# Performance work log

Hardware: AMD Instinct MI355X
Metric: run time of the kernel (lower is better)

Reference implementation:

```python
import jax, jax.numpy as jnp
import numpy as np

EMBED_DIM = 768
N_HEADS = 12
MLP_HID = 3072  # mlp_ratio 4.0
LN_EPS = 1e-6


def setup_inputs() -> dict:
    key = jax.random.key(0)
    ks = jax.random.split(key, 12)
    B, N, C = 4, 2048, EMBED_DIM
    s = 0.02
    return {
        "x": jax.random.normal(ks[0], (B, N, C), jnp.float32),
        "mask": jnp.ones((B, N), jnp.int32),
        "ln1_g": jnp.ones((C,), jnp.float32),
        "ln1_b": jnp.zeros((C,), jnp.float32),
        "qkv_w": jax.random.normal(ks[1], (C, 3 * C), jnp.float32) * s,
        "qkv_b": jnp.zeros((3 * C,), jnp.float32),
        "proj_w": jax.random.normal(ks[2], (C, C), jnp.float32) * s,
        "proj_b": jnp.zeros((C,), jnp.float32),
        "ln2_g": jnp.ones((C,), jnp.float32),
        "ln2_b": jnp.zeros((C,), jnp.float32),
        "fc1_w": jax.random.normal(ks[3], (C, MLP_HID), jnp.float32) * s,
        "fc1_b": jnp.zeros((MLP_HID,), jnp.float32),
        "fc2_w": jax.random.normal(ks[4], (MLP_HID, C), jnp.float32) * s,
        "fc2_b": jnp.zeros((C,), jnp.float32),
    }


def _layernorm(x, g, b):
    mu = jnp.mean(x, axis=-1, keepdims=True)
    var = jnp.mean(jnp.square(x - mu), axis=-1, keepdims=True)
    return (x - mu) * jax.lax.rsqrt(var + LN_EPS) * g + b


def _block(x, mask, ln1_g, ln1_b, qkv_w, qkv_b, proj_w, proj_b,
           ln2_g, ln2_b, fc1_w, fc1_b, fc2_w, fc2_b):
    B, N, C = x.shape
    H, D = N_HEADS, C // N_HEADS
    scale = D ** -0.5

    # --- attention (pre-norm) ---
    h = _layernorm(x, ln1_g, ln1_b)
    qkv = h @ qkv_w + qkv_b                      # [B,N,3C]
    qkv = qkv.reshape(B, N, 3, H, D).transpose(2, 0, 3, 1, 4)
    q, k, v = qkv[0], qkv[1], qkv[2]             # [B,H,N,D]
    scores = jnp.einsum("bhqd,bhkd->bhqk", q, k * scale)
    # 2-D mask path: (bsz, seq) -> (bsz, 1, seq, 1), mask queries
    m = mask[:, None, :, None]
    scores = jnp.where(m == 0, jnp.finfo(scores.dtype).min, scores)
    attn = jax.nn.softmax(scores, axis=-1)
    vals = jnp.einsum("bhqk,bhkd->bhqd", attn, v)
    vals = vals.transpose(0, 2, 1, 3).reshape(B, N, C)
    x = x + (vals @ proj_w + proj_b)

    # --- MLP (pre-norm, GELU exact) ---
    h = _layernorm(x, ln2_g, ln2_b)
    h = jax.nn.gelu(h @ fc1_w + fc1_b, approximate=False)
    x = x + (h @ fc2_w + fc2_b)
    return x


def reference(x, mask, ln1_g, ln1_b, qkv_w, qkv_b, proj_w, proj_b,
              ln2_g, ln2_b, fc1_w, fc1_b, fc2_w, fc2_b):
    return _block(x, mask, ln1_g, ln1_b, qkv_w, qkv_b, proj_w, proj_b,
                  ln2_g, ln2_b, fc1_w, fc1_b, fc2_w, fc2_b)
```

## Files before the change

### kernel.cpp

```cpp
#include <hip/hip_runtime.h>
#include <hip/hip_bf16.h>
#include <math.h>

using bf16 = __hip_bfloat16;
typedef short s16x8 __attribute__((ext_vector_type(8)));
typedef float f32x4 __attribute__((ext_vector_type(4)));
typedef float f32x16 __attribute__((ext_vector_type(16)));

#define LOG2E 1.4426950408889634f
#define QSCALE 0.18033688f

__device__ inline unsigned short f2bf(float f) {
    bf16 h = __float2bfloat16(f);
    return __builtin_bit_cast(unsigned short, h);
}

__device__ inline void gload_lds16(const void* g, void* l) {
    __builtin_amdgcn_global_load_lds(
        (const __attribute__((address_space(1))) void*)g,
        (__attribute__((address_space(3))) void*)l, 16, 0, 0);
}

__device__ inline float swap_halves(float x, int hi) {
    unsigned a = __builtin_bit_cast(unsigned, x);
    unsigned b = a;
    asm volatile("v_permlane32_swap_b32 %0, %1" : "+v"(a), "+v"(b));
    return hi ? __builtin_bit_cast(float, a) : __builtin_bit_cast(float, b);
}

__device__ inline unsigned cvtpk(float lo, float hi) {
    unsigned r;
    asm("v_cvt_pk_bf16_f32 %0, %1, %2" : "=v"(r) : "v"(lo), "v"(hi));
    return r;
}

__device__ inline s16x8 build_pfrag(float p0, float p1, float p2, float p3,
                                    float p4, float p5, float p6, float p7) {
    unsigned w01 = cvtpk(p0, p1);
    unsigned w23 = cvtpk(p2, p3);
    unsigned w45 = cvtpk(p4, p5);
    unsigned w67 = cvtpk(p6, p7);
    asm volatile("v_permlane32_swap_b32 %0, %1" : "+v"(w01), "+v"(w45));
    asm volatile("v_permlane32_swap_b32 %0, %1" : "+v"(w23), "+v"(w67));
    int4 t = {(int)w01, (int)w23, (int)w45, (int)w67};
    return __builtin_bit_cast(s16x8, t);
}

__global__ __launch_bounds__(256) void transpose_bf16(
    const float* __restrict__ in, bf16* __restrict__ out, int K, int N)
{
    __shared__ float tile[32][33];
    const int bx = blockIdx.x * 32;
    const int by = blockIdx.y * 32;
    const int tx = threadIdx.x, ty = threadIdx.y;
    #pragma unroll
    for (int i = 0; i < 32; i += 8)
        tile[ty + i][tx] = in[(size_t)(by + ty + i) * N + bx + tx];
    __syncthreads();
    #pragma unroll
    for (int i = 0; i < 32; i += 8)
        out[(size_t)(bx + ty + i) * K + by + tx] = __float2bfloat16(tile[tx][ty + i]);
}

__global__ __launch_bounds__(256) void ln_kernel(
    const float* __restrict__ x, const float* __restrict__ g,
    const float* __restrict__ bb, bf16* __restrict__ out)
{
    const int row = blockIdx.x;
    const float* xr = x + (size_t)row * 768;
    float v[3];
    float s = 0.f, s2 = 0.f;
    #pragma unroll
    for (int i = 0; i < 3; ++i) {
        v[i] = xr[threadIdx.x + i * 256];
        s += v[i];
        s2 += v[i] * v[i];
    }
    #pragma unroll
    for (int off = 1; off < 64; off <<= 1) {
        s += __shfl_xor(s, off);
        s2 += __shfl_xor(s2, off);
    }
    __shared__ float rs[4], rs2[4];
    const int wave = threadIdx.x >> 6;
    if ((threadIdx.x & 63) == 0) { rs[wave] = s; rs2[wave] = s2; }
    __syncthreads();
    s = rs[0] + rs[1] + rs[2] + rs[3];
    s2 = rs2[0] + rs2[1] + rs2[2] + rs2[3];
    const float mu = s * (1.f / 768.f);
    const float var = s2 * (1.f / 768.f) - mu * mu;
    const float r = rsqrtf(var + 1e-6f);
    bf16* orow = out + (size_t)row * 768;
    #pragma unroll
    for (int i = 0; i < 3; ++i) {
        const int col = threadIdx.x + i * 256;
        orow[col] = __float2bfloat16((v[i] - mu) * r * g[col] + bb[col]);
    }
}

#define BM 128
#define BN 128
#define BK 64

template <int EPI>
__global__ __launch_bounds__(256) void gemm_bt(
    const bf16* __restrict__ A, const bf16* __restrict__ Bt,
    const float* __restrict__ bias, const float* __restrict__ resid,
    void* __restrict__ outp, const int* __restrict__ mask,
    bf16* __restrict__ Qb, bf16* __restrict__ Kb, bf16* __restrict__ Vt,
    int M, int N, int K)
{
    __shared__ alignas(16) char smem[32768];
    char* As = smem;
    char* Bs = smem + 16384;
    const int tid = threadIdx.x;
    const int lane = tid & 63;
    const int wave = tid >> 6;
    const int wm = wave >> 1, wn = wave & 1;
    const int lr = lane & 15, lg = lane >> 4;
    const int bm = blockIdx.x, bn = blockIdx.y;

    f32x4 acc[4][4] = {};

    const size_t a_row0 = (size_t)bm * BM;
    const size_t b_row0 = (size_t)bn * BN;

    for (int kt = 0; kt < K; kt += BK) {
        #pragma unroll
        for (int i = 0; i < 4; ++i) {
            const int id = tid + i * 256;
            const int row = id >> 3, c = id & 7;
            const int cs = (c ^ (row & 7)) * 8;
            gload_lds16(A + (a_row0 + row) * K + kt + cs, As + id * 16);
            gload_lds16(Bt + (b_row0 + row) * K + kt + cs, Bs + id * 16);
        }
        __syncthreads();
        #pragma unroll
        for (int ks = 0; ks < 2; ++ks) {
            s16x8 af[4], bfr[4];
            #pragma unroll
            for (int mf = 0; mf < 4; ++mf) {
                const int row = wm * 64 + mf * 16 + lr;
                const int c = ks * 4 + lg;
                af[mf] = *reinterpret_cast<const s16x8*>(As + row * 128 + ((c ^ (row & 7)) * 16));
            }
            #pragma unroll
            for (int nf = 0; nf < 4; ++nf) {
                const int row = wn * 64 + nf * 16 + lr;
                const int c = ks * 4 + lg;
                bfr[nf] = *reinterpret_cast<const s16x8*>(Bs + row * 128 + ((c ^ (row & 7)) * 16));
            }
            #pragma unroll
            for (int mf = 0; mf < 4; ++mf)
                #pragma unroll
                for (int nf = 0; nf < 4; ++nf)
                    acc[mf][nf] = __builtin_amdgcn_mfma_f32_16x16x32_bf16(
                        af[mf], bfr[nf], acc[mf][nf], 0, 0, 0);
        }
        __syncthreads();
    }

    if (EPI == 3) {
        const int rq = bn / 6;
        const int bb_ = bm >> 4;
        if (rq == 2) {
            char* Ws = smem + wave * 8192;
            #pragma unroll
            for (int nf = 0; nf < 4; ++nf) {
                const int cl = nf * 16 + lr;
                const int gn = bn * 128 + wn * 64 + nf * 16 + lr;
                const float bs = bias[gn];
                #pragma unroll
                for (int mf = 0; mf < 4; ++mf) {
                    unsigned short pk[4];
                    #pragma unroll
                    for (int i = 0; i < 4; ++i) pk[i] = f2bf(acc[mf][nf][i] + bs);
                    const int slot = (2 * mf + (lg >> 1)) ^ (cl & 7);
                    *reinterpret_cast<long long*>(Ws + cl * 128 + slot * 16 + (lg & 1) * 8) =
                        *reinterpret_cast<const long long*>(pk);
                }
            }
            __syncthreads();
            const int nb = (bm * 128 + wm * 64) & 2047;
            const int cb = (bn - 12) * 128 + wn * 64;
            #pragma unroll
            for (int r = 0; r < 8; ++r) {
                const int cl = r * 8 + (lane >> 3);
                const int j = lane & 7;
                const int4 vv = *reinterpret_cast<const int4*>(
                    Ws + cl * 128 + ((j ^ (cl & 7)) * 16));
                const int c = cb + cl;
                const int hh = c >> 6, dd = c & 63;
                *reinterpret_cast<int4*>(
                    Vt + ((size_t)(bb_ * 12 + hh) * 64 + dd) * 2048 + nb + j * 8) = vv;
            }
        } else {
            const int cb = bn * 128 - rq * 768 + wn * 64;
            bf16* dst = (rq == 0) ? Qb : Kb;
            #pragma unroll
            for (int mf = 0; mf < 4; ++mf) {
                #pragma unroll
                for (int i = 0; i < 4; ++i) {
                    const int gm = bm * 128 + wm * 64 + mf * 16 + 4 * lg + i;
                    const int n = gm & 2047;
                    const float msc = (rq == 0) ? (mask[gm] ? QSCALE : 0.f) : 1.f;
                    #pragma unroll
                    for (int nf = 0; nf < 4; ++nf) {
                        const int c = cb + nf * 16 + lr;
                        const int h = c >> 6, d = c & 63;
                        const int gn = bn * 128 + wn * 64 + nf * 16 + lr;
                        const float v = (acc[mf][nf][i] + bias[gn]) * msc;
                        dst[((size_t)(bb_ * 12 + h) * 2048 + n) * 64 + d] =
                            __float2bfloat16(v);
                    }
                }
            }
        }
        return;
    }

    #pragma unroll
    for (int mf = 0; mf < 4; ++mf) {
        #pragma unroll
        for (int i = 0; i < 4; ++i) {
            const int gm = bm * BM + wm * 64 + mf * 16 + 4 * lg + i;
            #pragma unroll
            for (int nf = 0; nf < 4; ++nf) {
                const int gn = bn * BN + wn * 64 + nf * 16 + lr;
                float v = acc[mf][nf][i] + bias[gn];
                if (EPI == 1) v += resid[(size_t)gm * N + gn];
                if (EPI == 2) {
                    const float x3 = v * v * v;
                    const float z = fmaf(x3, 0.044715f, v) * 2.3022080f;
                    const float e = __builtin_amdgcn_exp2f(z);
                    v = v - v * __builtin_amdgcn_rcpf(1.f + e);
                }
                if (EPI == 1)
                    reinterpret_cast<float*>(outp)[(size_t)gm * N + gn] = v;
                else
                    reinterpret_cast<bf16*>(outp)[(size_t)gm * N + gn] = __float2bfloat16(v);
            }
        }
    }
}

__global__ __launch_bounds__(256, 3) void attn_kernel(
    const bf16* __restrict__ Qb, const bf16* __restrict__ Kb,
    const bf16* __restrict__ Vt, bf16* __restrict__ out)
{
    __shared__ alignas(16) char Ks[2][64 * 128];
    __shared__ alignas(16) char Vs[2][64 * 128];

    const int lin = blockIdx.x;
    const int xcd = lin & 7, slot = lin >> 3;
    const int pair = xcd * 6 + (slot >> 4);
    const int qb = slot & 15;
    const int b = pair / 12, h = pair % 12;

    const int tid = threadIdx.x, lane = tid & 63, wave = tid >> 6;
    const int lq = lane & 31;
    const int hi = lane >> 5;
    const size_t bh = (size_t)(b * 12 + h);
    const bf16* Kh = Kb + bh * 2048 * 64;
    const bf16* Vh = Vt + bh * 64 * 2048;
    const int q0w = qb * 128 + wave * 32;

    s16x8 qf[4];
    {
        const bf16* qp = Qb + (bh * 2048 + q0w + lq) * 64 + 8 * hi;
        #pragma unroll
        for (int ks = 0; ks < 4; ++ks)
            qf[ks] = *reinterpret_cast<const s16x8*>(qp + 16 * ks);
    }

    int sKoff0, sKoff1, dst0, dst1;
    size_t sVoff0, sVoff1;
    {
        const int id0 = tid;
        const int R0 = id0 >> 4;
        const int u0 = (id0 & 15) ^ (R0 & 15);
        const int rt0 = 2 * R0 + (u0 >> 3), s80 = (u0 & 7) * 8;
        sKoff0 = rt0 * 64 + s80;
        sVoff0 = (size_t)rt0 * 2048 + s80;
        dst0 = id0 * 16;
        const int id1 = tid + 256;
        const int R1 = id1 >> 4;
        const int u1 = (id1 & 15) ^ (R1 & 15);
        const int rt1 = 2 * R1 + (u1 >> 3), s81 = (u1 & 7) * 8;
        sKoff1 = rt1 * 64 + s81;
        sVoff1 = (size_t)rt1 * 2048 + s81;
        dst1 = id1 * 16;
    }

    const int rh = lq >> 1;
    const int m7 = rh & 7;
    const int rbase = rh * 256 + (((((lq & 1) << 3) ^ (rh & 8))) << 4);

    float l_r = 0.f;
    f32x16 o0 = {}, o1 = {};

    #define STAGE(buf, kb)                                                    \
        do {                                                                  \
            gload_lds16(Kh + (kb) * 4096 + sKoff0, Ks[buf] + dst0);           \
            gload_lds16(Vh + (kb) * 64 + sVoff0, Vs[buf] + dst0);             \
            gload_lds16(Kh + (kb) * 4096 + sKoff1, Ks[buf] + dst1);           \
            gload_lds16(Vh + (kb) * 64 + sVoff1, Vs[buf] + dst1);             \
        } while (0)

    STAGE(0, 0);
    __syncthreads();
    int cur = 0;

    for (int kb = 0; kb < 32; ++kb) {
        if (kb < 31) STAGE(cur ^ 1, kb + 1);
        const char* Kc = Ks[cur] + rbase;
        const char* Vc = Vs[cur] + rbase;

        f32x16 st0 = {}, st1 = {};
        __builtin_amdgcn_s_setprio(1);
        #pragma unroll
        for (int ks = 0; ks < 4; ++ks) {
            const int so = (((2 * ks + hi) ^ m7) << 4);
            const s16x8 kf0 = *reinterpret_cast<const s16x8*>(Kc + so);
            st0 = __builtin_amdgcn_mfma_f32_32x32x16_bf16(kf0, qf[ks], st0, 0, 0, 0);
            const s16x8 kf1 = *reinterpret_cast<const s16x8*>(Kc + 4096 + so);
            st1 = __builtin_amdgcn_mfma_f32_32x32x16_bf16(kf1, qf[ks], st1, 0, 0, 0);
        }
        __builtin_amdgcn_s_setprio(0);

        float p0[16], p1[16];
        float rsa = 0.f, rsb = 0.f;
        #pragma unroll
        for (int r = 0; r < 16; ++r) {
            p0[r] = __builtin_amdgcn_exp2f(st0[r]);
            p1[r] = __builtin_amdgcn_exp2f(st1[r]);
            rsa += p0[r];
            rsb += p1[r];
        }
        l_r += rsa + rsb;

        const s16x8 pf00 = build_pfrag(p0[0], p0[1], p0[2], p0[3], p0[4], p0[5], p0[6], p0[7]);
        const s16x8 pf01 = build_pfrag(p0[8], p0[9], p0[10], p0[11], p0[12], p0[13], p0[14], p0[15]);
        const s16x8 pf10 = build_pfrag(p1[0], p1[1], p1[2], p1[3], p1[4], p1[5], p1[6], p1[7]);
        const s16x8 pf11 = build_pfrag(p1[8], p1[9], p1[10], p1[11], p1[12], p1[13], p1[14], p1[15]);

        __builtin_amdgcn_s_setprio(1);
        #pragma unroll
        for (int kf4 = 0; kf4 < 4; ++kf4) {
            const s16x8 pf = (kf4 == 0) ? pf00 : (kf4 == 1) ? pf01
                           : (kf4 == 2) ? pf10 : pf11;
            const int so = (((2 * kf4 + hi) ^ m7) << 4);
            const s16x8 vf0 = *reinterpret_cast<const s16x8*>(Vc + so);
            o0 = __builtin_amdgcn_mfma_f32_32x32x16_bf16(vf0, pf, o0, 0, 0, 0);
            const s16x8 vf1 = *reinterpret_cast<const s16x8*>(Vc + 4096 + so);
            o1 = __builtin_amdgcn_mfma_f32_32x32x16_bf16(vf1, pf, o1, 0, 0, 0);
        }
        __builtin_amdgcn_s_setprio(0);

        __syncthreads();
        cur ^= 1;
    }
    #undef STAGE

    l_r += swap_halves(l_r, hi);

    const float rl = 1.0f / l_r;
    bf16* orow = out + (size_t)(b * 2048 + q0w + lq) * 768 + h * 64;
    #pragma unroll
    for (int g = 0; g < 4; ++g) {
        unsigned short pk0[4], pk1[4];
        #pragma unroll
        for (int i = 0; i < 4; ++i) {
            pk0[i] = f2bf(o0[4 * g + i] * rl);
            pk1[i] = f2bf(o1[4 * g + i] * rl);
        }
        const int d0 = 8 * g + 4 * hi;
        *reinterpret_cast<int2*>(orow + d0) = *reinterpret_cast<const int2*>(pk0);
        *reinterpret_cast<int2*>(orow + 32 + d0) = *reinterpret_cast<const int2*>(pk1);
    }
}

extern "C" void kernel_launch(void* const* d_in, const int* in_sizes, int n_in,
                              void* d_out, int out_size, void* d_ws, size_t ws_size,
                              hipStream_t stream)
{
    (void)in_sizes; (void)n_in; (void)out_size; (void)ws_size;
    const float* x      = (const float*)d_in[0];
    const int*   mask   = (const int*)d_in[1];
    const float* ln1_g  = (const float*)d_in[2];
    const float* ln1_b  = (const float*)d_in[3];
    const float* qkv_w  = (const float*)d_in[4];
    const float* qkv_b  = (const float*)d_in[5];
    const float* proj_w = (const float*)d_in[6];
    const float* proj_b = (const float*)d_in[7];
    const float* ln2_g  = (const float*)d_in[8];
    const float* ln2_b  = (const float*)d_in[9];
    const float* fc1_w  = (const float*)d_in[10];
    const float* fc1_b  = (const float*)d_in[11];
    const float* fc2_w  = (const float*)d_in[12];
    const float* fc2_b  = (const float*)d_in[13];
    float* out = (float*)d_out;
    char* ws = (char*)d_ws;

    bf16*  Wt_qkv  = (bf16*)(ws + 0);
    bf16*  Wt_proj = (bf16*)(ws + 3538944);
    bf16*  Wt_fc1  = (bf16*)(ws + 4718592);
    bf16*  Wt_fc2  = (bf16*)(ws + 9437184);
    bf16*  hbuf    = (bf16*)(ws + 14155776);
    bf16*  attnout = (bf16*)(ws + 64487424);
    float* x1      = (float*)(ws + 77070336);
    bf16*  h2      = (bf16*)(ws + 102236160);
    bf16*  a1      = (bf16*)(ws + 114819072);
    bf16*  Qb      = (bf16*)(ws + 114819072);
    bf16*  Kb      = (bf16*)(ws + 127401984);
    bf16*  Vt      = (bf16*)(ws + 139984896);

    const dim3 tb(32, 8);
    transpose_bf16<<<dim3(2304 / 32, 768 / 32), tb, 0, stream>>>(qkv_w, Wt_qkv, 768, 2304);
    transpose_bf16<<<dim3(768 / 32, 768 / 32), tb, 0, stream>>>(proj_w, Wt_proj, 768, 768);
    transpose_bf16<<<dim3(3072 / 32, 768 / 32), tb, 0, stream>>>(fc1_w, Wt_fc1, 768, 3072);
    transpose_bf16<<<dim3(768 / 32, 3072 / 32), tb, 0, stream>>>(fc2_w, Wt_fc2, 3072, 768);

    ln_kernel<<<8192, 256, 0, stream>>>(x, ln1_g, ln1_b, hbuf);
    gemm_bt<3><<<dim3(64, 18), 256, 0, stream>>>(hbuf, Wt_qkv, qkv_b, nullptr, nullptr,
                                                 mask, Qb, Kb, Vt, 8192, 2304, 768);
    attn_kernel<<<768, 256, 0, stream>>>(Qb, Kb, Vt, attnout);
    gemm_bt<1><<<dim3(64, 6), 256, 0, stream>>>(attnout, Wt_proj, proj_b, x, x1,
                                                nullptr, nullptr, nullptr, nullptr, 8192, 768, 768);
    ln_kernel<<<8192, 256, 0, stream>>>(x1, ln2_g, ln2_b, h2);
    gemm_bt<2><<<dim3(64, 24), 256, 0, stream>>>(h2, Wt_fc1, fc1_b, nullptr, a1,
                                                 nullptr, nullptr, nullptr, nullptr, 8192, 3072, 768);
    gemm_bt<1><<<dim3(64, 6), 256, 0, stream>>>(a1, Wt_fc2, fc2_b, x1, out,
                                                nullptr, nullptr, nullptr, nullptr, 8192, 768, 3072);
}
```

Baseline: 273.7 us.

## Use 64-row GEMM tiles for N=768 GEMMs, fuse transposes, MFMA row sums

```diff
diff --git a/kernel.cpp b/kernel.cpp
--- a/kernel.cpp
+++ b/kernel.cpp
@@ -19,13 +19,6 @@
     __builtin_amdgcn_global_load_lds(
         (const __attribute__((address_space(1))) void*)g,
         (__attribute__((address_space(3))) void*)l, 16, 0, 0);
-}
-
-__device__ inline float swap_halves(float x, int hi) {
-    unsigned a = __builtin_bit_cast(unsigned, x);
-    unsigned b = a;
-    asm volatile("v_permlane32_swap_b32 %0, %1" : "+v"(a), "+v"(b));
-    return hi ? __builtin_bit_cast(float, a) : __builtin_bit_cast(float, b);
 }
 
 __device__ inline unsigned cvtpk(float lo, float hi) {
@@ -46,12 +39,24 @@
     return __builtin_bit_cast(s16x8, t);
 }
 
-__global__ __launch_bounds__(256) void transpose_bf16(
-    const float* __restrict__ in, bf16* __restrict__ out, int K, int N)
+__global__ __launch_bounds__(256) void transpose_all(
+    const float* __restrict__ qkv_w, const float* __restrict__ proj_w,
+    const float* __restrict__ fc1_w, const float* __restrict__ fc2_w,
+    bf16* __restrict__ Wqkv, bf16* __restrict__ Wproj,
+    bf16* __restrict__ Wfc1, bf16* __restrict__ Wfc2)
 {
+    int t = blockIdx.x;
+    const float* in;
+    bf16* out;
+    int K, N, xt;
+    if (t < 1728)      { in = qkv_w;  out = Wqkv;  K = 768;  N = 2304; xt = 72; }
+    else if (t < 2304) { in = proj_w; out = Wproj; K = 768;  N = 768;  xt = 24; t -= 1728; }
+    else if (t < 4608) { in = fc1_w;  out = Wfc1;  K = 768;  N = 3072; xt = 96; t -= 2304; }
+    else               { in = fc2_w;  out = Wfc2;  K = 3072; N = 768;  xt = 24; t -= 4608; }
+    const int bx = (t % xt) * 32;
+    const int by = (t / xt) * 32;
+
     __shared__ float tile[32][33];
-    const int bx = blockIdx.x * 32;
-    const int by = blockIdx.y * 32;
     const int tx = threadIdx.x, ty = threadIdx.y;
     #pragma unroll
     for (int i = 0; i < 32; i += 8)
@@ -98,14 +103,10 @@
     }
 }
 
-#define BM 128
-#define BN 128
-#define BK 64
-
 template <int EPI>
 __global__ __launch_bounds__(256) void gemm_bt(
     const bf16* __restrict__ A, const bf16* __restrict__ Bt,
-    const float* __restrict__ bias, const float* __restrict__ resid,
+    const float* __restrict__ bias,
     void* __restrict__ outp, const int* __restrict__ mask,
     bf16* __restrict__ Qb, bf16* __restrict__ Kb, bf16* __restrict__ Vt,
     int M, int N, int K)
@@ -122,10 +123,10 @@
 
     f32x4 acc[4][4] = {};
 
-    const size_t a_row0 = (size_t)bm * BM;
-    const size_t b_row0 = (size_t)bn * BN;
-
-    for (int kt = 0; kt < K; kt += BK) {
+    const size_t a_row0 = (size_t)bm * 128;
+    const size_t b_row0 = (size_t)bn * 128;
+
+    for (int kt = 0; kt < K; kt += 64) {
         #pragma unroll
         for (int i = 0; i < 4; ++i) {
             const int id = tid + i * 256;
@@ -223,22 +224,93 @@
     for (int mf = 0; mf < 4; ++mf) {
         #pragma unroll
         for (int i = 0; i < 4; ++i) {
-            const int gm = bm * BM + wm * 64 + mf * 16 + 4 * lg + i;
+            const int gm = bm * 128 + wm * 64 + mf * 16 + 4 * lg + i;
             #pragma unroll
             for (int nf = 0; nf < 4; ++nf) {
-                const int gn = bn * BN + wn * 64 + nf * 16 + lr;
+                const int gn = bn * 128 + wn * 64 + nf * 16 + lr;
                 float v = acc[mf][nf][i] + bias[gn];
-                if (EPI == 1) v += resid[(size_t)gm * N + gn];
                 if (EPI == 2) {
                     const float x3 = v * v * v;
                     const float z = fmaf(x3, 0.044715f, v) * 2.3022080f;
                     const float e = __builtin_amdgcn_exp2f(z);
                     v = v - v * __builtin_amdgcn_rcpf(1.f + e);
                 }
-                if (EPI == 1)
-                    reinterpret_cast<float*>(outp)[(size_t)gm * N + gn] = v;
-                else
-                    reinterpret_cast<bf16*>(outp)[(size_t)gm * N + gn] = __float2bfloat16(v);
+                reinterpret_cast<bf16*>(outp)[(size_t)gm * N + gn] = __float2bfloat16(v);
+            }
+        }
+    }
+}
+
+__global__ __launch_bounds__(256) void gemm64(
+    const bf16* __restrict__ A, const bf16* __restrict__ Bt,
+    const float* __restrict__ bias, const float* __restrict__ resid,
+    float* __restrict__ outp, int M, int N, int K)
+{
+    __shared__ alignas(16) char smem[24576];
+    char* As = smem;
+    char* Bs = smem + 8192;
+    const int tid = threadIdx.x;
+    const int lane = tid & 63;
+    const int wn = tid >> 6;
+    const int lr = lane & 15, lg = lane >> 4;
+    const int bm = blockIdx.x, bn = blockIdx.y;
+
+    f32x4 acc[4][2] = {};
+
+    const size_t a_row0 = (size_t)bm * 64;
+    const size_t b_row0 = (size_t)bn * 128;
+
+    for (int kt = 0; kt < K; kt += 64) {
+        #pragma unroll
+        for (int i = 0; i < 2; ++i) {
+            const int id = tid + i * 256;
+            const int row = id >> 3, c = id & 7;
+            const int cs = (c ^ (row & 7)) * 8;
+            gload_lds16(A + (a_row0 + row) * K + kt + cs, As + id * 16);
+        }
+        #pragma unroll
+        for (int i = 0; i < 4; ++i) {
+            const int id = tid + i * 256;
+            const int row = id >> 3, c = id & 7;
+            const int cs = (c ^ (row & 7)) * 8;
+            gload_lds16(Bt + (b_row0 + row) * K + kt + cs, Bs + id * 16);
+        }
+        __syncthreads();
+        #pragma unroll
+        for (int ks = 0; ks < 2; ++ks) {
+            s16x8 af[4], bfr[2];
+            #pragma unroll
+            for (int mf = 0; mf < 4; ++mf) {
+                const int row = mf * 16 + lr;
+                const int c = ks * 4 + lg;
+                af[mf] = *reinterpret_cast<const s16x8*>(As + row * 128 + ((c ^ (row & 7)) * 16));
+            }
+            #pragma unroll
+            for (int nf = 0; nf < 2; ++nf) {
+                const int row = wn * 32 + nf * 16 + lr;
+                const int c = ks * 4 + lg;
+                bfr[nf] = *reinterpret_cast<const s16x8*>(Bs + row * 128 + ((c ^ (row & 7)) * 16));
+            }
+            #pragma unroll
+            for (int mf = 0; mf < 4; ++mf)
+                #pragma unroll
+                for (int nf = 0; nf < 2; ++nf)
+                    acc[mf][nf] = __builtin_amdgcn_mfma_f32_16x16x32_bf16(
+                        af[mf], bfr[nf], acc[mf][nf], 0, 0, 0);
+        }
+        __syncthreads();
+    }
+
+    #pragma unroll
+    for (int mf = 0; mf < 4; ++mf) {
+        #pragma unroll
+        for (int i = 0; i < 4; ++i) {
+            const int gm = bm * 64 + mf * 16 + 4 * lg + i;
+            #pragma unroll
+            for (int nf = 0; nf < 2; ++nf) {
+                const int gn = bn * 128 + wn * 32 + nf * 16 + lr;
+                outp[(size_t)gm * N + gn] =
+                    acc[mf][nf][i] + bias[gn] + resid[(size_t)gm * N + gn];
             }
         }
     }
@@ -272,6 +344,8 @@
         for (int ks = 0; ks < 4; ++ks)
             qf[ks] = *reinterpret_cast<const s16x8*>(qp + 16 * ks);
     }
+    const int4 onesw = {0x3F803F80, 0x3F803F80, 0x3F803F80, 0x3F803F80};
+    const s16x8 onesf = __builtin_bit_cast(s16x8, onesw);
 
     int sKoff0, sKoff1, dst0, dst1;
     size_t sVoff0, sVoff1;
@@ -296,8 +370,8 @@
     const int m7 = rh & 7;
     const int rbase = rh * 256 + (((((lq & 1) << 3) ^ (rh & 8))) << 4);
 
-    float l_r = 0.f;
     f32x16 o0 = {}, o1 = {};
+    f32x16 os = {};
 
     #define STAGE(buf, kb)                                                    \
         do {                                                                  \
@@ -329,15 +403,11 @@
         __builtin_amdgcn_s_setprio(0);
 
         float p0[16], p1[16];
-        float rsa = 0.f, rsb = 0.f;
         #pragma unroll
         for (int r = 0; r < 16; ++r) {
             p0[r] = __builtin_amdgcn_exp2f(st0[r]);
             p1[r] = __builtin_amdgcn_exp2f(st1[r]);
-            rsa += p0[r];
-            rsb += p1[r];
-        }
-        l_r += rsa + rsb;
+        }
 
         const s16x8 pf00 = build_pfrag(p0[0], p0[1], p0[2], p0[3], p0[4], p0[5], p0[6], p0[7]);
         const s16x8 pf01 = build_pfrag(p0[8], p0[9], p0[10], p0[11], p0[12], p0[13], p0[14], p0[15]);
@@ -354,6 +424,7 @@
             o0 = __builtin_amdgcn_mfma_f32_32x32x16_bf16(vf0, pf, o0, 0, 0, 0);
             const s16x8 vf1 = *reinterpret_cast<const s16x8*>(Vc + 4096 + so);
             o1 = __builtin_amdgcn_mfma_f32_32x32x16_bf16(vf1, pf, o1, 0, 0, 0);
+            os = __builtin_amdgcn_mfma_f32_32x32x16_bf16(onesf, pf, os, 0, 0, 0);
         }
         __builtin_amdgcn_s_setprio(0);
 
@@ -362,9 +433,7 @@
     }
     #undef STAGE
 
-    l_r += swap_halves(l_r, hi);
-
-    const float rl = 1.0f / l_r;
+    const float rl = 1.0f / os[0];
     bf16* orow = out + (size_t)(b * 2048 + q0w + lq) * 768 + h * 64;
     #pragma unroll
     for (int g = 0; g < 4; ++g) {
@@ -415,21 +484,18 @@
     bf16*  Kb      = (bf16*)(ws + 127401984);
     bf16*  Vt      = (bf16*)(ws + 139984896);
 
-    const dim3 tb(32, 8);
-    transpose_bf16<<<dim3(2304 / 32, 768 / 32), tb, 0, stream>>>(qkv_w, Wt_qkv, 768, 2304);
-    transpose_bf16<<<dim3(768 / 32, 768 / 32), tb, 0, stream>>>(proj_w, Wt_proj, 768, 768);
-    transpose_bf16<<<dim3(3072 / 32, 768 / 32), tb, 0, stream>>>(fc1_w, Wt_fc1, 768, 3072);
-    transpose_bf16<<<dim3(768 / 32, 3072 / 32), tb, 0, stream>>>(fc2_w, Wt_fc2, 3072, 768);
+    transpose_all<<<6912, dim3(32, 8), 0, stream>>>(
+        qkv_w, proj_w, fc1_w, fc2_w, Wt_qkv, Wt_proj, Wt_fc1, Wt_fc2);
 
     ln_kernel<<<8192, 256, 0, stream>>>(x, ln1_g, ln1_b, hbuf);
-    gemm_bt<3><<<dim3(64, 18), 256, 0, stream>>>(hbuf, Wt_qkv, qkv_b, nullptr, nullptr,
+    gemm_bt<3><<<dim3(64, 18), 256, 0, stream>>>(hbuf, Wt_qkv, qkv_b, nullptr,
                                                  mask, Qb, Kb, Vt, 8192, 2304, 768);
     attn_kernel<<<768, 256, 0, stream>>>(Qb, Kb, Vt, attnout);
-    gemm_bt<1><<<dim3(64, 6), 256, 0, stream>>>(attnout, Wt_proj, proj_b, x, x1,
-                                                nullptr, nullptr, nullptr, nullptr, 8192, 768, 768);
+    gemm64<<<dim3(128, 6), 256, 0, stream>>>(attnout, Wt_proj, proj_b, x, x1,
+                                             8192, 768, 768);
     ln_kernel<<<8192, 256, 0, stream>>>(x1, ln2_g, ln2_b, h2);
-    gemm_bt<2><<<dim3(64, 24), 256, 0, stream>>>(h2, Wt_fc1, fc1_b, nullptr, a1,
+    gemm_bt<2><<<dim3(64, 24), 256, 0, stream>>>(h2, Wt_fc1, fc1_b, a1,
                                                  nullptr, nullptr, nullptr, nullptr, 8192, 3072, 768);
-    gemm_bt<1><<<dim3(64, 6), 256, 0, stream>>>(a1, Wt_fc2, fc2_b, x1, out,
-                                                nullptr, nullptr, nullptr, nullptr, 8192, 768, 3072);
-}
+    gemm64<<<dim3(128, 6), 256, 0, stream>>>(a1, Wt_fc2, fc2_b, x1, out,
+                                             8192, 768, 3072);
+}
```

Result: faster. 252.3 us (-7.8%).
